# Optimization experiments

Measured on AMD Instinct MI355X. Metric: run time of the kernel, lower is better.

## Reference

```python
import jax, jax.numpy as jnp
import numpy as np

N_NODES = 50000
N_EDGES = 500000
D_FEAT = 128
HIDDEN = 128
EPS = 1e-8


def _lin_init(key, fan_in, fan_out):
    return jax.random.normal(key, (fan_in, fan_out), dtype=jnp.float32) / np.sqrt(fan_in)


def setup_inputs() -> dict:
    key = jax.random.key(0)
    ks = jax.random.split(key, 16)
    h = jax.random.normal(ks[0], (N_NODES, D_FEAT), dtype=jnp.float32)
    coord = jax.random.normal(ks[1], (N_NODES, 3), dtype=jnp.float32)
    vel = jax.random.normal(ks[2], (N_NODES, 3), dtype=jnp.float32)
    edge_index = jax.random.randint(ks[3], (2, N_EDGES), 0, N_NODES, dtype=jnp.int32)
    return {
        "h": h, "coord": coord, "vel": vel, "edge_index": edge_index,
        "W_e1": _lin_init(ks[4], 2 * D_FEAT + 1, HIDDEN), "b_e1": jnp.zeros((HIDDEN,), jnp.float32),
        "W_e2": _lin_init(ks[5], HIDDEN, D_FEAT), "b_e2": jnp.zeros((D_FEAT,), jnp.float32),
        "W_c1": _lin_init(ks[6], D_FEAT, HIDDEN), "b_c1": jnp.zeros((HIDDEN,), jnp.float32),
        "W_c2": _lin_init(ks[7], HIDDEN, 1), "b_c2": jnp.zeros((1,), jnp.float32),
        "W_v1": _lin_init(ks[8], D_FEAT, HIDDEN), "b_v1": jnp.zeros((HIDDEN,), jnp.float32),
        "W_v2": _lin_init(ks[9], HIDDEN, 1), "b_v2": jnp.zeros((1,), jnp.float32),
        "W_n1": _lin_init(ks[10], 2 * D_FEAT, HIDDEN), "b_n1": jnp.zeros((HIDDEN,), jnp.float32),
        "W_n2": _lin_init(ks[11], HIDDEN, D_FEAT), "b_n2": jnp.zeros((D_FEAT,), jnp.float32),
    }


def reference(h, coord, vel, edge_index,
              W_e1, b_e1, W_e2, b_e2,
              W_c1, b_c1, W_c2, b_c2,
              W_v1, b_v1, W_v2, b_v2,
              W_n1, b_n1, W_n2, b_n2):
    act = jax.nn.silu
    r, c = edge_index[0], edge_index[1]
    n = coord.shape[0]

    # coord2radial with normalize=True
    diff = coord[r] - coord[c]                      # [E, 3]
    rad = jnp.sum(diff * diff, axis=-1, keepdims=True)  # [E, 1]
    norm = jnp.sqrt(jax.lax.stop_gradient(rad)) + EPS
    diff = diff / norm

    # edge_op: Linear -> act -> Linear -> act
    edge_in = jnp.concatenate([h[r], h[c], rad], axis=1)  # [E, 2D+1]
    m_ij = act(act(edge_in @ W_e1 + b_e1) @ W_e2 + b_e2)  # [E, D]

    # coord_op: Linear -> act -> Linear (scalar weight per edge)
    weights = act(m_ij @ W_c1 + b_c1) @ W_c2 + b_c2       # [E, 1]
    coors_sum = jax.ops.segment_sum(diff * weights, r, num_segments=n)  # [N, 3]

    # vel_op: Linear -> act -> Linear (scalar per node)
    vel_weights = act(h @ W_v1 + b_v1) @ W_v2 + b_v2      # [N, 1]
    coord_out = coord + coors_sum + vel * vel_weights

    # node aggregation + node_op: Linear -> act -> Linear
    m_i = jax.ops.segment_sum(m_ij, r, num_segments=h.shape[0])  # [N, D]
    agg = jnp.concatenate([h, m_i], axis=1)               # [N, 2D]
    h_out = act(agg @ W_n1 + b_n1) @ W_n2 + b_n2          # [N, D]
    return (h_out, coord_out)
```

## Files before the change

kernel.cpp:

```cpp
#include <hip/hip_runtime.h>
#include <stdint.h>

#define NN 50000
#define NE 500000
#define NEB ((NE + 127) / 128)
#define SST 136

#define BARRIER() asm volatile("s_waitcnt lgkmcnt(0)\n\ts_barrier" ::: "memory")
#define WAVE_SYNC() asm volatile("s_waitcnt lgkmcnt(0)" ::: "memory")

typedef __attribute__((ext_vector_type(8))) short bf16x8;
typedef __attribute__((ext_vector_type(4))) float f32x4;

__device__ __forceinline__ float silu(float x) {
    float e = __expf(-x);
    return x * __builtin_amdgcn_rcpf(1.0f + e);
}
__device__ __forceinline__ float bf2f(unsigned short s) {
    union { unsigned int u; float f; } v; v.u = ((unsigned int)s) << 16; return v.f;
}
__device__ __forceinline__ float bflo(unsigned int u) {
    union { unsigned int u; float f; } v; v.u = u << 16; return v.f;
}
__device__ __forceinline__ float bfhi(unsigned int u) {
    union { unsigned int u; float f; } v; v.u = u & 0xffff0000u; return v.f;
}
__device__ __forceinline__ unsigned short f2bf(float f) {
    union { float f; unsigned int u; } v; v.f = f;
    return (unsigned short)((v.u + 0x7fffu + ((v.u >> 16) & 1u)) >> 16);
}
__device__ __forceinline__ unsigned int pack2(float a, float b) {
    unsigned int r;
    asm("v_cvt_pk_bf16_f32 %0, %1, %2" : "=v"(r) : "v"(a), "v"(b));
    return r;
}
__device__ __forceinline__ bf16x8 packf8(const float* p) {
    float4 f0 = *(const float4*)p; float4 f1 = *(const float4*)(p + 4);
    union { bf16x8 v; unsigned int u[4]; } o;
    o.u[0] = pack2(f0.x, f0.y); o.u[1] = pack2(f0.z, f0.w);
    o.u[2] = pack2(f1.x, f1.y); o.u[3] = pack2(f1.z, f1.w);
    return o.v;
}

__global__ void prep_h(const float* __restrict__ h, unsigned short* __restrict__ hb) {
    int i = blockIdx.x * 256 + threadIdx.x;
    if (i < NN * 128 / 4) {
        float4 v = ((const float4*)h)[i];
        uint2 o; o.x = pack2(v.x, v.y); o.y = pack2(v.z, v.w);
        ((uint2*)hb)[i] = o;
    }
}

__global__ void prep_w(const float* __restrict__ We1, const float* __restrict__ We2,
                       const float* __restrict__ Wc1, const float* __restrict__ Wv1,
                       const float* __restrict__ Wn1, const float* __restrict__ Wn2,
                       unsigned short* __restrict__ Wt1, unsigned short* __restrict__ Wt2,
                       unsigned short* __restrict__ Wt3, unsigned short* __restrict__ Wv1t,
                       unsigned short* __restrict__ Wn1t, unsigned short* __restrict__ Wn2t) {
    int i = blockIdx.x * 256 + threadIdx.x;
    if (i < 32768) {
        int j = i >> 8, k = i & 255;
        Wt1[i] = f2bf(We1[k * 128 + j]);
    } else if (i < 49152) {
        int t = i - 32768; int j = t >> 7, ks = t & 127;
        int k0 = (ks & 7) * 16 + (ks >> 3);
        Wt2[t] = f2bf(We2[k0 * 128 + j]);
    } else if (i < 65536) {
        int t = i - 49152; int j = t >> 7, ks = t & 127;
        int k0 = (ks & 7) * 16 + (ks >> 3);
        Wt3[t] = f2bf(Wc1[k0 * 128 + j]);
    } else if (i < 81920) {
        int t = i - 65536; int j = t >> 7, k = t & 127;
        Wv1t[t] = f2bf(Wv1[k * 128 + j]);
    } else if (i < 114688) {
        int t = i - 81920; int j = t >> 8, k = t & 255;
        int ksrc;
        if (k < 128) ksrc = k;
        else { int ks = k - 128; ksrc = 128 + (ks & 7) * 16 + (ks >> 3); }
        Wn1t[t] = f2bf(Wn1[ksrc * 128 + j]);
    } else if (i < 131072) {
        int t = i - 114688; int j = t >> 7, ks = t & 127;
        int k0 = (ks & 7) * 16 + (ks >> 3);
        Wn2t[t] = f2bf(Wn2[k0 * 128 + j]);
    }
}

__global__ void csr_count(const int* __restrict__ eidx, int* __restrict__ deg) {
    int e = blockIdx.x * 256 + threadIdx.x;
    if (e < NE) atomicAdd(&deg[eidx[e]], 1);
}

__global__ void scan_a(const int* __restrict__ deg, int* __restrict__ bsum) {
    __shared__ int s[256];
    int t = threadIdx.x, idx = blockIdx.x * 256 + t;
    s[t] = (idx < NN) ? deg[idx] : 0;
    __syncthreads();
    for (int off = 128; off > 0; off >>= 1) {
        if (t < off) s[t] += s[t + off];
        __syncthreads();
    }
    if (t == 0) bsum[blockIdx.x] = s[0];
}

__global__ void scan_b(int* __restrict__ bsum) {
    __shared__ int s[256];
    int t = threadIdx.x;
    int v = (t < 196) ? bsum[t] : 0;
    s[t] = v;
    __syncthreads();
    for (int off = 1; off < 256; off <<= 1) {
        int x = (t >= off) ? s[t - off] : 0;
        __syncthreads();
        s[t] += x;
        __syncthreads();
    }
    if (t < 196) bsum[t] = s[t] - v;
}

__global__ void scan_c(const int* __restrict__ deg, const int* __restrict__ bsum,
                       int* __restrict__ rowptr) {
    __shared__ int s[256];
    int t = threadIdx.x, idx = blockIdx.x * 256 + t;
    int v = (idx < NN) ? deg[idx] : 0;
    s[t] = v;
    __syncthreads();
    for (int off = 1; off < 256; off <<= 1) {
        int x = (t >= off) ? s[t - off] : 0;
        __syncthreads();
        s[t] += x;
        __syncthreads();
    }
    if (idx < NN) rowptr[idx] = bsum[blockIdx.x] + s[t] - v;
    if (idx == 0) rowptr[NN] = NE;
}

__global__ void csr_fill(const int* __restrict__ eidx, const int* __restrict__ rowptr,
                         int* __restrict__ cursor,
                         int* __restrict__ csr_r, int* __restrict__ csr_c) {
    int e = blockIdx.x * 256 + threadIdx.x;
    if (e < NE) {
        int r = eidx[e], c = eidx[NE + e];
        int slot = rowptr[r] + atomicAdd(&cursor[r], 1);
        csr_r[slot] = r; csr_c[slot] = c;
    }
}

__device__ __forceinline__ void stage256(const unsigned short* __restrict__ W, int halfk,
                                         unsigned short* sW, int tid) {
#pragma unroll
    for (int t = 0; t < 8; ++t) {
        int idx = tid + t * 256; int j = idx >> 4, g = idx & 15;
        *(uint4*)(sW + j * SST + g * 8) = *(const uint4*)(W + (size_t)j * 256 + halfk * 128 + g * 8);
    }
}
__device__ __forceinline__ void stage128(const unsigned short* __restrict__ W,
                                         unsigned short* sW, int tid) {
#pragma unroll
    for (int t = 0; t < 8; ++t) {
        int idx = tid + t * 256; int j = idx >> 4, g = idx & 15;
        *(uint4*)(sW + j * SST + g * 8) = *(const uint4*)(W + (size_t)j * 128 + g * 8);
    }
}
__device__ __forceinline__ void mfma4(const bf16x8 a[2][4], const unsigned short* sW,
                                      int l16, int q, f32x4 acc[2][8]) {
#pragma unroll
    for (int kc = 0; kc < 4; ++kc)
#pragma unroll
        for (int ct = 0; ct < 8; ++ct) {
            bf16x8 b = *(const bf16x8*)(sW + (ct * 16 + l16) * SST + kc * 32 + q * 8);
            acc[0][ct] = __builtin_amdgcn_mfma_f32_16x16x32_bf16(a[0][kc], b, acc[0][ct], 0, 0, 0);
            acc[1][ct] = __builtin_amdgcn_mfma_f32_16x16x32_bf16(a[1][kc], b, acc[1][ct], 0, 0, 0);
        }
}

__global__ __launch_bounds__(256, 2) void prep_P(
    const unsigned short* __restrict__ hb,
    const unsigned short* __restrict__ Wt1,
    unsigned short* __restrict__ P1, unsigned short* __restrict__ P2)
{
    __shared__ __align__(16) unsigned short sWa[128 * SST];
    __shared__ __align__(16) unsigned short sWb[128 * SST];
    const int tid = threadIdx.x;
    const int wv = tid >> 6, lane = tid & 63, q = lane >> 4, l16 = lane & 15;
    const int n0 = blockIdx.x * 128;

    stage256(Wt1, 0, sWa, tid);
    stage256(Wt1, 1, sWb, tid);
    bf16x8 ah[2][4];
#pragma unroll
    for (int si = 0; si < 2; ++si) {
        int nn = n0 + (wv * 2 + si) * 16 + l16; if (nn >= NN) nn = NN - 1;
#pragma unroll
        for (int kc = 0; kc < 4; ++kc)
            ah[si][kc] = *(const bf16x8*)(hb + (size_t)nn * 128 + kc * 32 + q * 8);
    }
    BARRIER();

    f32x4 acc[2][8];
#pragma unroll
    for (int si = 0; si < 2; ++si)
#pragma unroll
        for (int ct = 0; ct < 8; ++ct) acc[si][ct] = (f32x4){0.f, 0.f, 0.f, 0.f};
    mfma4(ah, sWa, l16, q, acc);
#pragma unroll
    for (int si = 0; si < 2; ++si)
#pragma unroll
        for (int r = 0; r < 4; ++r) {
            int n = n0 + (wv * 2 + si) * 16 + q * 4 + r;
            if (n < NN) {
                uint4 pk = make_uint4(pack2(acc[si][0][r], acc[si][1][r]),
                                      pack2(acc[si][2][r], acc[si][3][r]),
                                      pack2(acc[si][4][r], acc[si][5][r]),
                                      pack2(acc[si][6][r], acc[si][7][r]));
                *(uint4*)(P1 + (size_t)n * 128 + l16 * 8) = pk;
            }
        }
#pragma unroll
    for (int si = 0; si < 2; ++si)
#pragma unroll
        for (int ct = 0; ct < 8; ++ct) acc[si][ct] = (f32x4){0.f, 0.f, 0.f, 0.f};
    mfma4(ah, sWb, l16, q, acc);
#pragma unroll
    for (int si = 0; si < 2; ++si)
#pragma unroll
        for (int r = 0; r < 4; ++r) {
            int n = n0 + (wv * 2 + si) * 16 + q * 4 + r;
            if (n < NN) {
                uint4 pk = make_uint4(pack2(acc[si][0][r], acc[si][1][r]),
                                      pack2(acc[si][2][r], acc[si][3][r]),
                                      pack2(acc[si][4][r], acc[si][5][r]),
                                      pack2(acc[si][6][r], acc[si][7][r]));
                *(uint4*)(P2 + (size_t)n * 128 + l16 * 8) = pk;
            }
        }
}

__global__ __launch_bounds__(256, 2) void egcl_edge(
    const float* __restrict__ coord,
    const int* __restrict__ csr_r, const int* __restrict__ csr_c,
    const unsigned short* __restrict__ P1, const unsigned short* __restrict__ P2,
    const unsigned short* __restrict__ Wt2, const unsigned short* __restrict__ Wt3,
    const float* __restrict__ We1,
    const float* __restrict__ be1, const float* __restrict__ be2,
    const float* __restrict__ bc1,
    const float* __restrict__ Wc2, const float* __restrict__ bc2,
    float* __restrict__ m_acc, float* __restrict__ c_sum)
{
    __shared__ __align__(16) unsigned short sM[128 * SST];
    __shared__ __align__(16) unsigned short sB3[128 * SST];
    __shared__ float sRad[128], sDif[128][3];
    __shared__ int sSeg[128];
    __shared__ float sWlS[128], sBe1S[128], sBe2[128], sBc1[128], sWc2f[128];

    const int tid = threadIdx.x;
    const int wv = tid >> 6, lane = tid & 63, q = lane >> 4, l16 = lane & 15;
    const int e0 = blockIdx.x * 128;

    int nr[2], nc[2];
#pragma unroll
    for (int si = 0; si < 2; ++si) {
        int e = e0 + (wv * 2 + si) * 16 + l16;
        if (e >= NE) e = NE - 1;
        nr[si] = csr_r[e]; nc[si] = csr_c[e];
    }
    bf16x8 pr[2][4], pc[2][4];
#pragma unroll
    for (int si = 0; si < 2; ++si)
#pragma unroll
        for (int kc = 0; kc < 4; ++kc) {
            pr[si][kc] = *(const bf16x8*)(P1 + (size_t)nr[si] * 128 + kc * 32 + q * 8);
            pc[si][kc] = *(const bf16x8*)(P2 + (size_t)nc[si] * 128 + kc * 32 + q * 8);
        }

    if (tid < 128) {
        int k0 = (tid & 7) * 16 + (tid >> 3);
        sWlS[tid] = We1[256 * 128 + k0]; sBe1S[tid] = be1[k0];
        sBe2[tid] = be2[tid]; sBc1[tid] = bc1[tid]; sWc2f[tid] = Wc2[tid];
        int s = e0 + tid; int sc = (s < NE) ? s : (NE - 1);
        int r = csr_r[sc], c = csr_c[sc];
        sSeg[tid] = (s < NE) ? r : -1;
        float dx = coord[r * 3 + 0] - coord[c * 3 + 0];
        float dy = coord[r * 3 + 1] - coord[c * 3 + 1];
        float dz = coord[r * 3 + 2] - coord[c * 3 + 2];
        float rad = fmaf(dx, dx, fmaf(dy, dy, dz * dz));
        float inv = 1.0f / (sqrtf(rad) + 1e-8f);
        sRad[tid] = rad;
        sDif[tid][0] = dx * inv; sDif[tid][1] = dy * inv; sDif[tid][2] = dz * inv;
    }
    stage128(Wt2, sM, tid);
    stage128(Wt3, sB3, tid);
    const float bc2v = bc2[0];
    BARRIER();

    bf16x8 a[2][4];
#pragma unroll
    for (int si = 0; si < 2; ++si) {
        int row = (wv * 2 + si) * 16 + l16;
        float rad = sRad[row];
#pragma unroll
        for (int kc = 0; kc < 4; ++kc) {
            const float* wl = sWlS + kc * 32 + q * 8;
            const float* be = sBe1S + kc * 32 + q * 8;
            union { bf16x8 v; unsigned int u[4]; } R, C;
            R.v = pr[si][kc]; C.v = pc[si][kc];
            float t[8];
#pragma unroll
            for (int p = 0; p < 4; ++p) {
                t[2 * p]     = bflo(R.u[p]) + bflo(C.u[p]);
                t[2 * p + 1] = bfhi(R.u[p]) + bfhi(C.u[p]);
            }
#pragma unroll
            for (int j = 0; j < 8; ++j)
                t[j] = silu(fmaf(rad, wl[j], t[j] + be[j]));
            union { bf16x8 v; unsigned int u[4]; } O;
            O.u[0] = pack2(t[0], t[1]); O.u[1] = pack2(t[2], t[3]);
            O.u[2] = pack2(t[4], t[5]); O.u[3] = pack2(t[6], t[7]);
            a[si][kc] = O.v;
        }
    }

    f32x4 acc[2][8];
#pragma unroll
    for (int si = 0; si < 2; ++si)
#pragma unroll
        for (int ct = 0; ct < 8; ++ct) acc[si][ct] = (f32x4){0.f, 0.f, 0.f, 0.f};
    mfma4(a, sM, l16, q, acc);
    uint4 mu[2][4];
#pragma unroll
    for (int si = 0; si < 2; ++si)
#pragma unroll
        for (int r = 0; r < 4; ++r) {
            float v[8];
#pragma unroll
            for (int ct = 0; ct < 8; ++ct) v[ct] = silu(acc[si][ct][r] + sBe2[ct * 16 + l16]);
            mu[si][r] = make_uint4(pack2(v[0], v[1]), pack2(v[2], v[3]),
                                   pack2(v[4], v[5]), pack2(v[6], v[7]));
        }
    BARRIER();
#pragma unroll
    for (int si = 0; si < 2; ++si)
#pragma unroll
        for (int r = 0; r < 4; ++r) {
            int row = (wv * 2 + si) * 16 + q * 4 + r;
            *(uint4*)(sM + row * SST + l16 * 8) = mu[si][r];
        }
    WAVE_SYNC();

#pragma unroll
    for (int si = 0; si < 2; ++si)
#pragma unroll
        for (int ct = 0; ct < 8; ++ct) acc[si][ct] = (f32x4){0.f, 0.f, 0.f, 0.f};
    {
        bf16x8 am[2][4];
#pragma unroll
        for (int si = 0; si < 2; ++si) {
            int row = (wv * 2 + si) * 16 + l16;
#pragma unroll
            for (int kc = 0; kc < 4; ++kc)
                am[si][kc] = *(const bf16x8*)(sM + row * SST + kc * 32 + q * 8);
        }
        mfma4(am, sB3, l16, q, acc);
    }
#pragma unroll
    for (int si = 0; si < 2; ++si) {
        float p[4];
#pragma unroll
        for (int r = 0; r < 4; ++r) {
            float s = 0.f;
#pragma unroll
            for (int ct = 0; ct < 8; ++ct) {
                int col = ct * 16 + l16;
                float t = silu(acc[si][ct][r] + sBc1[col]);
                s = fmaf(t, sWc2f[col], s);
            }
            p[r] = s;
        }
#pragma unroll
        for (int m = 1; m < 16; m <<= 1)
#pragma unroll
            for (int r = 0; r < 4; ++r) p[r] += __shfl_xor(p[r], m, 16);
        if (l16 == 0) {
#pragma unroll
            for (int r = 0; r < 4; ++r) {
                int row = (wv * 2 + si) * 16 + q * 4 + r;
                int rn = sSeg[row];
                if (rn >= 0) {
                    float wgt = p[r] + bc2v;
                    atomicAdd(&c_sum[(size_t)rn * 3 + 0], sDif[row][0] * wgt);
                    atomicAdd(&c_sum[(size_t)rn * 3 + 1], sDif[row][1] * wgt);
                    atomicAdd(&c_sum[(size_t)rn * 3 + 2], sDif[row][2] * wgt);
                }
            }
        }
    }
    BARRIER();

    {
        int p = tid & 127, half = tid >> 7;
        int base = half * 64;
        float run = 0.f;
        int cur = sSeg[base];
        bool openL = true;
#pragma unroll 1
        for (int i0 = 0; i0 < 64; i0 += 4) {
            float v[4]; int rr[4];
#pragma unroll
            for (int j = 0; j < 4; ++j) {
                int row = base + i0 + j;
                rr[j] = sSeg[row];
                v[j] = bf2f(sM[row * SST + p]);
            }
#pragma unroll
            for (int j = 0; j < 4; ++j) {
                if (rr[j] != cur) {
                    if (cur >= 0) {
                        float* dst = &m_acc[(size_t)cur * 128 + p];
                        if (openL) atomicAdd(dst, run);
                        else       *dst = run;
                    }
                    run = 0.f; cur = rr[j]; openL = false;
                }
                run += v[j];
            }
        }
        if (cur >= 0) atomicAdd(&m_acc[(size_t)cur * 128 + p], run);
    }
}

__global__ __launch_bounds__(256, 3) void egcl_node(
    const unsigned short* __restrict__ hb,
    const float* __restrict__ coord,
    const float* __restrict__ vel,
    const unsigned short* __restrict__ Wv1t, const float* __restrict__ bv1,
    const float* __restrict__ Wv2, const float* __restrict__ bv2,
    const unsigned short* __restrict__ Wn1t, const float* __restrict__ bn1,
    const unsigned short* __restrict__ Wn2t, const float* __restrict__ bn2,
    const float* __restrict__ m_acc, const float* __restrict__ c_sum,
    float* __restrict__ out_h, float* __restrict__ out_c)
{
    __shared__ __align__(16) unsigned short sAb[128 * SST];
    __shared__ float sBv1[128], sWv2f[128], sBn1[128], sBn2[128];

    const int tid = threadIdx.x;
    const int wv = tid >> 6, lane = tid & 63, q = lane >> 4, l16 = lane & 15;
    const int n0 = blockIdx.x * 128;
    int nval = NN - n0; if (nval > 128) nval = 128;

    if (tid < 128) {
        sBv1[tid] = bv1[tid]; sWv2f[tid] = Wv2[tid];
        sBn1[tid] = bn1[tid]; sBn2[tid] = bn2[tid];
    }
    const float bv2v = bv2[0];

    bf16x8 ah[2][4], am[2][4];
#pragma unroll
    for (int si = 0; si < 2; ++si) {
        int row = (wv * 2 + si) * 16 + l16;
        int nn = n0 + row; if (nn >= NN) nn = NN - 1;
#pragma unroll
        for (int kc = 0; kc < 4; ++kc) {
            ah[si][kc] = *(const bf16x8*)(hb + (size_t)nn * 128 + kc * 32 + q * 8);
            am[si][kc] = packf8(m_acc + (size_t)nn * 128 + kc * 32 + q * 8);
        }
    }

    BARRIER();

    f32x4 acc[2][8];
#pragma unroll
    for (int si = 0; si < 2; ++si)
#pragma unroll
        for (int ct = 0; ct < 8; ++ct) acc[si][ct] = (f32x4){0.f, 0.f, 0.f, 0.f};
#pragma unroll
    for (int kc = 0; kc < 4; ++kc)
#pragma unroll
        for (int ct = 0; ct < 8; ++ct) {
            bf16x8 b = *(const bf16x8*)(Wv1t + (size_t)(ct * 16 + l16) * 128 + kc * 32 + q * 8);
            acc[0][ct] = __builtin_amdgcn_mfma_f32_16x16x32_bf16(ah[0][kc], b, acc[0][ct], 0, 0, 0);
            acc[1][ct] = __builtin_amdgcn_mfma_f32_16x16x32_bf16(ah[1][kc], b, acc[1][ct], 0, 0, 0);
        }
#pragma unroll
    for (int si = 0; si < 2; ++si) {
        float p[4];
#pragma unroll
        for (int r = 0; r < 4; ++r) {
            float s = 0.f;
#pragma unroll
            for (int ct = 0; ct < 8; ++ct) {
                int col = ct * 16 + l16;
                float t = silu(acc[si][ct][r] + sBv1[col]);
                s = fmaf(t, sWv2f[col], s);
            }
            p[r] = s;
        }
#pragma unroll
        for (int m = 1; m < 16; m <<= 1)
#pragma unroll
            for (int r = 0; r < 4; ++r) p[r] += __shfl_xor(p[r], m, 16);
        if (l16 == 0) {
#pragma unroll
            for (int r = 0; r < 4; ++r) {
                int row = (wv * 2 + si) * 16 + q * 4 + r;
                int n = n0 + row;
                if (row < nval) {
                    float vw = p[r] + bv2v;
#pragma unroll
                    for (int d = 0; d < 3; ++d) {
                        float cv = coord[(size_t)n * 3 + d] + c_sum[(size_t)n * 3 + d]
                                 + vel[(size_t)n * 3 + d] * vw;
                        out_c[(size_t)n * 3 + d] = cv;
                    }
                }
            }
        }
    }

#pragma unroll
    for (int si = 0; si < 2; ++si)
#pragma unroll
        for (int ct = 0; ct < 8; ++ct) acc[si][ct] = (f32x4){0.f, 0.f, 0.f, 0.f};
#pragma unroll
    for (int kc = 0; kc < 8; ++kc)
#pragma unroll
        for (int ct = 0; ct < 8; ++ct) {
            bf16x8 b = *(const bf16x8*)(Wn1t + (size_t)(ct * 16 + l16) * 256 + kc * 32 + q * 8);
            bf16x8 a0 = (kc < 4) ? ah[0][kc & 3] : am[0][kc & 3];
            bf16x8 a1 = (kc < 4) ? ah[1][kc & 3] : am[1][kc & 3];
            acc[0][ct] = __builtin_amdgcn_mfma_f32_16x16x32_bf16(a0, b, acc[0][ct], 0, 0, 0);
            acc[1][ct] = __builtin_amdgcn_mfma_f32_16x16x32_bf16(a1, b, acc[1][ct], 0, 0, 0);
        }
#pragma unroll
    for (int si = 0; si < 2; ++si)
#pragma unroll
        for (int r = 0; r < 4; ++r) {
            int row = (wv * 2 + si) * 16 + q * 4 + r;
            float v[8];
#pragma unroll
            for (int ct = 0; ct < 8; ++ct) v[ct] = silu(acc[si][ct][r] + sBn1[ct * 16 + l16]);
            uint4 pk = make_uint4(pack2(v[0], v[1]), pack2(v[2], v[3]),
                                  pack2(v[4], v[5]), pack2(v[6], v[7]));
            *(uint4*)(sAb + row * SST + l16 * 8) = pk;
        }

    BARRIER();

#pragma unroll
    for (int si = 0; si < 2; ++si)
#pragma unroll
        for (int ct = 0; ct < 8; ++ct) acc[si][ct] = (f32x4){0.f, 0.f, 0.f, 0.f};
    {
        bf16x8 a[2][4];
#pragma unroll
        for (int si = 0; si < 2; ++si) {
            int row = (wv * 2 + si) * 16 + l16;
#pragma unroll
            for (int kc = 0; kc < 4; ++kc)
                a[si][kc] = *(const bf16x8*)(sAb + row * SST + kc * 32 + q * 8);
        }
#pragma unroll
        for (int kc = 0; kc < 4; ++kc)
#pragma unroll
            for (int ct = 0; ct < 8; ++ct) {
                bf16x8 b = *(const bf16x8*)(Wn2t + (size_t)(ct * 16 + l16) * 128 + kc * 32 + q * 8);
                acc[0][ct] = __builtin_amdgcn_mfma_f32_16x16x32_bf16(a[0][kc], b, acc[0][ct], 0, 0, 0);
                acc[1][ct] = __builtin_amdgcn_mfma_f32_16x16x32_bf16(a[1][kc], b, acc[1][ct], 0, 0, 0);
            }
    }
#pragma unroll
    for (int si = 0; si < 2; ++si)
#pragma unroll
        for (int r = 0; r < 4; ++r) {
            int row = (wv * 2 + si) * 16 + q * 4 + r;
            if (row < nval) {
                float* orow = out_h + (size_t)(n0 + row) * 128;
#pragma unroll
                for (int ct = 0; ct < 8; ++ct)
                    orow[ct * 16 + l16] = acc[si][ct][r] + sBn2[ct * 16 + l16];
            }
        }
}

extern "C" void kernel_launch(void* const* d_in, const int* in_sizes, int n_in,
                              void* d_out, int out_size, void* d_ws, size_t ws_size,
                              hipStream_t stream) {
    const float* h     = (const float*)d_in[0];
    const float* coord = (const float*)d_in[1];
    const float* vel   = (const float*)d_in[2];
    const int*   eidx  = (const int*)d_in[3];
    const float* We1 = (const float*)d_in[4];
    const float* be1 = (const float*)d_in[5];
    const float* We2 = (const float*)d_in[6];
    const float* be2 = (const float*)d_in[7];
    const float* Wc1 = (const float*)d_in[8];
    const float* bc1 = (const float*)d_in[9];
    const float* Wc2 = (const float*)d_in[10];
    const float* bc2 = (const float*)d_in[11];
    const float* Wv1 = (const float*)d_in[12];
    const float* bv1 = (const float*)d_in[13];
    const float* Wv2 = (const float*)d_in[14];
    const float* bv2 = (const float*)d_in[15];
    const float* Wn1 = (const float*)d_in[16];
    const float* bn1 = (const float*)d_in[17];
    const float* Wn2 = (const float*)d_in[18];
    const float* bn2 = (const float*)d_in[19];

    char* ws = (char*)d_ws;
    float* m_acc = (float*)ws;
    float* c_sum = (float*)(ws + 25600000);
    unsigned short* hb   = (unsigned short*)(ws + 26200064);
    unsigned short* Wt1  = (unsigned short*)(ws + 39000064);
    unsigned short* Wt2  = (unsigned short*)(ws + 39065600);
    unsigned short* Wt3  = (unsigned short*)(ws + 39098368);
    unsigned short* Wv1t = (unsigned short*)(ws + 39131136);
    unsigned short* Wn1t = (unsigned short*)(ws + 39163904);
    unsigned short* Wn2t = (unsigned short*)(ws + 39229440);
    int* deg    = (int*)(ws + 39262208);
    int* cursor = (int*)(ws + 39462208);
    int* rowptr = (int*)(ws + 39662208);
    int* bsum   = (int*)(ws + 39862272);
    int* csr_r  = (int*)(ws + 39863296);
    int* csr_c  = (int*)(ws + 41863296);
    unsigned short* P1 = (unsigned short*)(ws + 43863296);
    unsigned short* P2 = (unsigned short*)(ws + 56663296);

    hipMemsetAsync(ws, 0, 26200000, stream);
    hipMemsetAsync(ws + 39262208, 0, 400000, stream);

    prep_h<<<6250, 256, 0, stream>>>(h, hb);
    prep_w<<<512, 256, 0, stream>>>(We1, We2, Wc1, Wv1, Wn1, Wn2,
                                    Wt1, Wt2, Wt3, Wv1t, Wn1t, Wn2t);
    prep_P<<<(NN + 127) / 128, 256, 0, stream>>>(hb, Wt1, P1, P2);

    csr_count<<<1954, 256, 0, stream>>>(eidx, deg);
    scan_a<<<196, 256, 0, stream>>>(deg, bsum);
    scan_b<<<1, 256, 0, stream>>>(bsum);
    scan_c<<<196, 256, 0, stream>>>(deg, bsum, rowptr);
    csr_fill<<<1954, 256, 0, stream>>>(eidx, rowptr, cursor, csr_r, csr_c);

    egcl_edge<<<NEB, 256, 0, stream>>>(
        coord, csr_r, csr_c, P1, P2, Wt2, Wt3,
        We1, be1, be2, bc1, Wc2, bc2, m_acc, c_sum);

    float* out_h = (float*)d_out;
    float* out_c = out_h + (size_t)NN * 128;
    egcl_node<<<(NN + 127) / 128, 256, 0, stream>>>(
        hb, coord, vel, Wv1t, bv1, Wv2, bv2, Wn1t, bn1, Wn2t, bn2,
        m_acc, c_sum, out_h, out_c);
}
```

Baseline: 389.0 us.

## Merge prep and CSR kernels, fold scan stages, pack CSR row/col pairs

```diff
diff --git a/kernel.cpp b/kernel.cpp
--- a/kernel.cpp
+++ b/kernel.cpp
@@ -42,52 +42,51 @@
     return o.v;
 }
 
-__global__ void prep_h(const float* __restrict__ h, unsigned short* __restrict__ hb) {
-    int i = blockIdx.x * 256 + threadIdx.x;
-    if (i < NN * 128 / 4) {
+__global__ void prep_all(const float* __restrict__ h, unsigned short* __restrict__ hb,
+                         const float* __restrict__ We1, const float* __restrict__ We2,
+                         const float* __restrict__ Wc1, const float* __restrict__ Wv1,
+                         const float* __restrict__ Wn1, const float* __restrict__ Wn2,
+                         unsigned short* __restrict__ Wt1, unsigned short* __restrict__ Wt2,
+                         unsigned short* __restrict__ Wt3, unsigned short* __restrict__ Wv1t,
+                         unsigned short* __restrict__ Wn1t, unsigned short* __restrict__ Wn2t,
+                         const int* __restrict__ eidx, int* __restrict__ deg) {
+    int b = blockIdx.x, tid = threadIdx.x;
+    if (b < 6250) {
+        int i = b * 256 + tid;
         float4 v = ((const float4*)h)[i];
         uint2 o; o.x = pack2(v.x, v.y); o.y = pack2(v.z, v.w);
         ((uint2*)hb)[i] = o;
-    }
-}
-
-__global__ void prep_w(const float* __restrict__ We1, const float* __restrict__ We2,
-                       const float* __restrict__ Wc1, const float* __restrict__ Wv1,
-                       const float* __restrict__ Wn1, const float* __restrict__ Wn2,
-                       unsigned short* __restrict__ Wt1, unsigned short* __restrict__ Wt2,
-                       unsigned short* __restrict__ Wt3, unsigned short* __restrict__ Wv1t,
-                       unsigned short* __restrict__ Wn1t, unsigned short* __restrict__ Wn2t) {
-    int i = blockIdx.x * 256 + threadIdx.x;
-    if (i < 32768) {
-        int j = i >> 8, k = i & 255;
-        Wt1[i] = f2bf(We1[k * 128 + j]);
-    } else if (i < 49152) {
-        int t = i - 32768; int j = t >> 7, ks = t & 127;
-        int k0 = (ks & 7) * 16 + (ks >> 3);
-        Wt2[t] = f2bf(We2[k0 * 128 + j]);
-    } else if (i < 65536) {
-        int t = i - 49152; int j = t >> 7, ks = t & 127;
-        int k0 = (ks & 7) * 16 + (ks >> 3);
-        Wt3[t] = f2bf(Wc1[k0 * 128 + j]);
-    } else if (i < 81920) {
-        int t = i - 65536; int j = t >> 7, k = t & 127;
-        Wv1t[t] = f2bf(Wv1[k * 128 + j]);
-    } else if (i < 114688) {
-        int t = i - 81920; int j = t >> 8, k = t & 255;
-        int ksrc;
-        if (k < 128) ksrc = k;
-        else { int ks = k - 128; ksrc = 128 + (ks & 7) * 16 + (ks >> 3); }
-        Wn1t[t] = f2bf(Wn1[ksrc * 128 + j]);
-    } else if (i < 131072) {
-        int t = i - 114688; int j = t >> 7, ks = t & 127;
-        int k0 = (ks & 7) * 16 + (ks >> 3);
-        Wn2t[t] = f2bf(Wn2[k0 * 128 + j]);
-    }
-}
-
-__global__ void csr_count(const int* __restrict__ eidx, int* __restrict__ deg) {
-    int e = blockIdx.x * 256 + threadIdx.x;
-    if (e < NE) atomicAdd(&deg[eidx[e]], 1);
+    } else if (b < 6762) {
+        int i = (b - 6250) * 256 + tid;
+        if (i < 32768) {
+            int j = i >> 8, k = i & 255;
+            Wt1[i] = f2bf(We1[k * 128 + j]);
+        } else if (i < 49152) {
+            int t = i - 32768; int j = t >> 7, ks = t & 127;
+            int k0 = (ks & 7) * 16 + (ks >> 3);
+            Wt2[t] = f2bf(We2[k0 * 128 + j]);
+        } else if (i < 65536) {
+            int t = i - 49152; int j = t >> 7, ks = t & 127;
+            int k0 = (ks & 7) * 16 + (ks >> 3);
+            Wt3[t] = f2bf(Wc1[k0 * 128 + j]);
+        } else if (i < 81920) {
+            int t = i - 65536; int j = t >> 7, k = t & 127;
+            Wv1t[t] = f2bf(Wv1[k * 128 + j]);
+        } else if (i < 114688) {
+            int t = i - 81920; int j = t >> 8, k = t & 255;
+            int ksrc;
+            if (k < 128) ksrc = k;
+            else { int ks = k - 128; ksrc = 128 + (ks & 7) * 16 + (ks >> 3); }
+            Wn1t[t] = f2bf(Wn1[ksrc * 128 + j]);
+        } else if (i < 131072) {
+            int t = i - 114688; int j = t >> 7, ks = t & 127;
+            int k0 = (ks & 7) * 16 + (ks >> 3);
+            Wn2t[t] = f2bf(Wn2[k0 * 128 + j]);
+        }
+    } else {
+        int e = (b - 6762) * 256 + tid;
+        if (e < NE) atomicAdd(&deg[eidx[e]], 1);
+    }
 }
 
 __global__ void scan_a(const int* __restrict__ deg, int* __restrict__ bsum) {
@@ -102,25 +101,18 @@
     if (t == 0) bsum[blockIdx.x] = s[0];
 }
 
-__global__ void scan_b(int* __restrict__ bsum) {
+__global__ void scan_c2(const int* __restrict__ deg, const int* __restrict__ bsum,
+                        int* __restrict__ rowptr) {
+    __shared__ int sb[256];
     __shared__ int s[256];
-    int t = threadIdx.x;
-    int v = (t < 196) ? bsum[t] : 0;
-    s[t] = v;
+    int t = threadIdx.x, b = blockIdx.x, idx = b * 256 + t;
+    sb[t] = (t < b) ? bsum[t] : 0;
     __syncthreads();
-    for (int off = 1; off < 256; off <<= 1) {
-        int x = (t >= off) ? s[t - off] : 0;
+    for (int off = 128; off > 0; off >>= 1) {
+        if (t < off) sb[t] += sb[t + off];
         __syncthreads();
-        s[t] += x;
-        __syncthreads();
-    }
-    if (t < 196) bsum[t] = s[t] - v;
-}
-
-__global__ void scan_c(const int* __restrict__ deg, const int* __restrict__ bsum,
-                       int* __restrict__ rowptr) {
-    __shared__ int s[256];
-    int t = threadIdx.x, idx = blockIdx.x * 256 + t;
+    }
+    int base = sb[0];
     int v = (idx < NN) ? deg[idx] : 0;
     s[t] = v;
     __syncthreads();
@@ -130,18 +122,17 @@
         s[t] += x;
         __syncthreads();
     }
-    if (idx < NN) rowptr[idx] = bsum[blockIdx.x] + s[t] - v;
+    if (idx < NN) rowptr[idx] = base + s[t] - v;
     if (idx == 0) rowptr[NN] = NE;
 }
 
 __global__ void csr_fill(const int* __restrict__ eidx, const int* __restrict__ rowptr,
-                         int* __restrict__ cursor,
-                         int* __restrict__ csr_r, int* __restrict__ csr_c) {
+                         int* __restrict__ deg, int2* __restrict__ csr_rc) {
     int e = blockIdx.x * 256 + threadIdx.x;
     if (e < NE) {
         int r = eidx[e], c = eidx[NE + e];
-        int slot = rowptr[r] + atomicAdd(&cursor[r], 1);
-        csr_r[slot] = r; csr_c[slot] = c;
+        int slot = rowptr[r] + atomicSub(&deg[r], 1) - 1;
+        csr_rc[slot] = make_int2(r, c);
     }
 }
 
@@ -237,7 +228,7 @@
 
 __global__ __launch_bounds__(256, 2) void egcl_edge(
     const float* __restrict__ coord,
-    const int* __restrict__ csr_r, const int* __restrict__ csr_c,
+    const int2* __restrict__ csr_rc,
     const unsigned short* __restrict__ P1, const unsigned short* __restrict__ P2,
     const unsigned short* __restrict__ Wt2, const unsigned short* __restrict__ Wt3,
     const float* __restrict__ We1,
@@ -261,7 +252,8 @@
     for (int si = 0; si < 2; ++si) {
         int e = e0 + (wv * 2 + si) * 16 + l16;
         if (e >= NE) e = NE - 1;
-        nr[si] = csr_r[e]; nc[si] = csr_c[e];
+        int2 rc = csr_rc[e];
+        nr[si] = rc.x; nc[si] = rc.y;
     }
     bf16x8 pr[2][4], pc[2][4];
 #pragma unroll
@@ -277,7 +269,8 @@
         sWlS[tid] = We1[256 * 128 + k0]; sBe1S[tid] = be1[k0];
         sBe2[tid] = be2[tid]; sBc1[tid] = bc1[tid]; sWc2f[tid] = Wc2[tid];
         int s = e0 + tid; int sc = (s < NE) ? s : (NE - 1);
-        int r = csr_r[sc], c = csr_c[sc];
+        int2 rc = csr_rc[sc];
+        int r = rc.x, c = rc.y;
         sSeg[tid] = (s < NE) ? r : -1;
         float dx = coord[r * 3 + 0] - coord[c * 3 + 0];
         float dy = coord[r * 3 + 1] - coord[c * 3 + 1];
@@ -615,30 +608,26 @@
     unsigned short* Wn1t = (unsigned short*)(ws + 39163904);
     unsigned short* Wn2t = (unsigned short*)(ws + 39229440);
     int* deg    = (int*)(ws + 39262208);
-    int* cursor = (int*)(ws + 39462208);
     int* rowptr = (int*)(ws + 39662208);
     int* bsum   = (int*)(ws + 39862272);
-    int* csr_r  = (int*)(ws + 39863296);
-    int* csr_c  = (int*)(ws + 41863296);
+    int2* csr_rc = (int2*)(ws + 39863296);
     unsigned short* P1 = (unsigned short*)(ws + 43863296);
     unsigned short* P2 = (unsigned short*)(ws + 56663296);
 
     hipMemsetAsync(ws, 0, 26200000, stream);
-    hipMemsetAsync(ws + 39262208, 0, 400000, stream);
-
-    prep_h<<<6250, 256, 0, stream>>>(h, hb);
-    prep_w<<<512, 256, 0, stream>>>(We1, We2, Wc1, Wv1, Wn1, Wn2,
-                                    Wt1, Wt2, Wt3, Wv1t, Wn1t, Wn2t);
+    hipMemsetAsync(deg, 0, 200000, stream);
+
+    prep_all<<<8716, 256, 0, stream>>>(h, hb, We1, We2, Wc1, Wv1, Wn1, Wn2,
+                                       Wt1, Wt2, Wt3, Wv1t, Wn1t, Wn2t,
+                                       eidx, deg);
     prep_P<<<(NN + 127) / 128, 256, 0, stream>>>(hb, Wt1, P1, P2);
 
-    csr_count<<<1954, 256, 0, stream>>>(eidx, deg);
     scan_a<<<196, 256, 0, stream>>>(deg, bsum);
-    scan_b<<<1, 256, 0, stream>>>(bsum);
-    scan_c<<<196, 256, 0, stream>>>(deg, bsum, rowptr);
-    csr_fill<<<1954, 256, 0, stream>>>(eidx, rowptr, cursor, csr_r, csr_c);
+    scan_c2<<<196, 256, 0, stream>>>(deg, bsum, rowptr);
+    csr_fill<<<1954, 256, 0, stream>>>(eidx, rowptr, deg, csr_rc);
 
     egcl_edge<<<NEB, 256, 0, stream>>>(
-        coord, csr_r, csr_c, P1, P2, Wt2, Wt3,
+        coord, csr_rc, P1, P2, Wt2, Wt3,
         We1, be1, be2, bc1, Wc2, bc2, m_acc, c_sum);
 
     float* out_h = (float*)d_out;
```

Result: faster. 375.1 us (-3.6%).
